# Kernel tuning notes

Measured on AMD Instinct MI355X. Metric: run time of the kernel, lower is better.

Reference implementation:

```python
import jax, jax.numpy as jnp
import numpy as np

D = 128; N_CELLS = 512; N_GENES = 256; HEADS = 4; HD = D // HEADS
E_SP = 8192; E_GRN = 2048

def _ln(x, g, b):
    m = jnp.mean(x, -1, keepdims=True)
    v = jnp.var(x, -1, keepdims=True)
    return (x - m) * jax.lax.rsqrt(v + 1e-5) * g + b

def setup_inputs():
    key = jax.random.key(0)
    ks = jax.random.split(key, 16)
    w = lambda i, shp: jax.random.normal(ks[i], shp, jnp.float32) * 0.02
    return {
        "high_emb": jax.random.normal(ks[0], (N_CELLS, D), jnp.float32),
        "low_emb": jax.random.normal(ks[1], (N_CELLS, N_GENES, D), jnp.float32),
        "spatial_edge_index": jax.random.randint(ks[2], (2, E_SP), 0, N_CELLS),
        "grn_edge_index": jax.random.randint(ks[3], (2, E_GRN), 0, N_GENES),
        "gin_w1": w(4, (D, 2 * D)), "gin_b1": jnp.zeros((2 * D,)),
        "gin_w2": w(5, (2 * D, D)), "gin_b2": jnp.zeros((D,)),
        "gin_eps": jnp.zeros(()),
        "gin_ln_g": jnp.ones((D,)), "gin_ln_b": jnp.zeros((D,)),
        "tc_wq": w(6, (D, D)), "tc_bq": jnp.zeros((D,)),
        "tc_wk": w(7, (D, D)), "tc_bk": jnp.zeros((D,)),
        "tc_wv": w(8, (D, D)), "tc_bv": jnp.zeros((D,)),
        "tc_wskip": w(9, (D, D)), "tc_bskip": jnp.zeros((D,)),
        "tc_ln_g": jnp.ones((D,)), "tc_ln_b": jnp.zeros((D,)),
        "cross_w": w(10, (6, D, D)), "cross_b": jnp.zeros((6, D)),
        "agg_w": w(11, (D, D)), "agg_b": jnp.zeros((D,)),
        "nh_g": jnp.ones((D,)), "nh_b": jnp.zeros((D,)),
        "nl_g": jnp.ones((D,)), "nl_b": jnp.zeros((D,)),
    }

def _forward(high_emb, low_emb, spatial_edge_index, grn_edge_index,
             gin_w1, gin_b1, gin_w2, gin_b2, gin_eps, gin_ln_g, gin_ln_b,
             tc_wq, tc_bq, tc_wk, tc_bk, tc_wv, tc_bv, tc_wskip, tc_bskip,
             tc_ln_g, tc_ln_b, cross_w, cross_b, agg_w, agg_b,
             nh_g, nh_b, nl_g, nl_b):
    # ---- high level: GIN conv over spatial cell graph ----
    s_src, s_dst = spatial_edge_index[0], spatial_edge_index[1]
    agg = jax.ops.segment_sum(high_emb[s_src], s_dst, num_segments=N_CELLS)
    h = (1.0 + gin_eps) * high_emb + agg
    h = jax.nn.gelu(h @ gin_w1 + gin_b1, approximate=False) @ gin_w2 + gin_b2
    high_out = _ln(h, gin_ln_g, gin_ln_b)

    # ---- low level: TransformerConv on per-cell GRN (edge structure shared across cells) ----
    g_src, g_dst = grn_edge_index[0], grn_edge_index[1]
    q = (low_emb @ tc_wq + tc_bq).reshape(N_CELLS, N_GENES, HEADS, HD)
    k = (low_emb @ tc_wk + tc_bk).reshape(N_CELLS, N_GENES, HEADS, HD)
    v = (low_emb @ tc_wv + tc_bv).reshape(N_CELLS, N_GENES, HEADS, HD)
    # per-edge attention logits, edge axis leading for segment ops: (E, C, H)
    logits = jnp.einsum('cehd,cehd->ech', q[:, g_dst], k[:, g_src]) / np.sqrt(HD).astype(np.float32)
    mx = jax.lax.stop_gradient(jax.ops.segment_max(logits, g_dst, num_segments=N_GENES))
    ex = jnp.exp(logits - mx[g_dst])
    den = jax.ops.segment_sum(ex, g_dst, num_segments=N_GENES)
    alpha = ex / den[g_dst]                          # (E, C, H) softmax per target gene
    v_s = jnp.moveaxis(v[:, g_src], 0, 1)            # (E, C, H, HD)
    out = jax.ops.segment_sum(alpha[..., None] * v_s, g_dst, num_segments=N_GENES)
    out = jnp.moveaxis(out, 0, 1).reshape(N_CELLS, N_GENES, D)
    out = out + low_emb @ tc_wskip + tc_bskip        # PyG root_weight skip
    low_out = _ln(out, tc_ln_g, tc_ln_b)

    # ---- gene aggregation + cross-level sigmoid gating ----
    gene_agg = jax.nn.gelu(jnp.mean(low_out, axis=1) @ agg_w + agg_b, approximate=False)
    scale = D ** -0.5
    q1 = high_out @ cross_w[0] + cross_b[0]
    k1 = gene_agg @ cross_w[1] + cross_b[1]
    v1 = gene_agg @ cross_w[2] + cross_b[2]
    high_cross = jax.nn.sigmoid(jnp.sum(q1 * k1, -1, keepdims=True) * scale) * v1
    q2 = gene_agg @ cross_w[3] + cross_b[3]
    k2 = high_out @ cross_w[4] + cross_b[4]
    v2 = high_out @ cross_w[5] + cross_b[5]
    low_cross = jax.nn.sigmoid(jnp.sum(q2 * k2, -1, keepdims=True) * scale) * v2

    high_new = _ln(high_emb + high_out + high_cross, nh_g, nh_b)
    low_new = _ln(low_emb + low_out + low_cross[:, None, :], nl_g, nl_b)
    return (high_new, low_new)

def reference(high_emb, low_emb, spatial_edge_index, grn_edge_index,
              gin_w1, gin_b1, gin_w2, gin_b2, gin_eps, gin_ln_g, gin_ln_b,
              tc_wq, tc_bq, tc_wk, tc_bk, tc_wv, tc_bv, tc_wskip, tc_bskip,
              tc_ln_g, tc_ln_b, cross_w, cross_b, agg_w, agg_b,
              nh_g, nh_b, nl_g, nl_b):
    return _forward(high_emb, low_emb, spatial_edge_index, grn_edge_index,
                    gin_w1, gin_b1, gin_w2, gin_b2, gin_eps, gin_ln_g, gin_ln_b,
                    tc_wq, tc_bq, tc_wk, tc_bk, tc_wv, tc_bv, tc_wskip, tc_bskip,
                    tc_ln_g, tc_ln_b, cross_w, cross_b, agg_w, agg_b,
                    nh_g, nh_b, nl_g, nl_b)
```

## Files before the change

### kernel.cpp

```cpp
#include <hip/hip_runtime.h>
#include <hip/hip_bf16.h>
#include <math.h>

#define N_CELLS 512
#define N_GENES 256
#define D 128
#define HEADS 4
#define HD 32
#define E_SP 8192
#define E_GRN 2048

typedef __attribute__((ext_vector_type(8))) short bf16x8;
typedef __attribute__((ext_vector_type(4))) float f32x4;


__device__ __forceinline__ float gelu_exact(float x) {
    return 0.5f * x * (1.0f + erff(x * 0.70710678118654752f));
}

__device__ __forceinline__ unsigned short f2bf(float f) {
    unsigned u = __float_as_uint(f);
    return (unsigned short)((u + 0x7FFFu + ((u >> 16) & 1u)) >> 16);
}

__device__ __forceinline__ float blo(unsigned u) { return __uint_as_float(u << 16); }
__device__ __forceinline__ float bhi(unsigned u) { return __uint_as_float(u & 0xFFFF0000u); }
__device__ __forceinline__ float bdot(unsigned a, unsigned b) {
    return blo(a) * blo(b) + bhi(a) * bhi(b);
}

template<int NT>
__device__ __forceinline__ float blockSum(float v, float* sbuf) {
    #pragma unroll
    for (int off = 32; off > 0; off >>= 1) v += __shfl_down(v, off, 64);
    int lane = threadIdx.x & 63, wid = threadIdx.x >> 6;
    __syncthreads();
    if (lane == 0) sbuf[wid] = v;
    __syncthreads();
    float r = 0.f;
    #pragma unroll
    for (int i = 0; i < NT / 64; ++i) r += sbuf[i];
    return r;
}


__global__ void gin_scatter_kernel(const float* __restrict__ high,
                                   const int* __restrict__ sp,
                                   float* __restrict__ agg) {
    int tid = blockIdx.x * 256 + threadIdx.x;
    int e = tid >> 7, d = tid & 127;
    int src = sp[e], dst = sp[E_SP + e];
    atomicAdd(&agg[dst * D + d], high[src * D + d]);
}

__global__ __launch_bounds__(256) void gin_mlp_kernel(
    const float* __restrict__ high, const float* __restrict__ agg,
    const float* __restrict__ eps,
    const float* __restrict__ w1, const float* __restrict__ b1,
    const float* __restrict__ w2, const float* __restrict__ b2,
    const float* __restrict__ lng, const float* __restrict__ lnb,
    float* __restrict__ high_out) {
    int c = blockIdx.x;
    int t = threadIdx.x;
    __shared__ float h[D];
    __shared__ float h1[2 * D];
    __shared__ float sbuf[4];
    if (t < D) h[t] = (1.f + eps[0]) * high[c * D + t] + agg[c * D + t];
    __syncthreads();
    float a = b1[t];
    for (int k = 0; k < D; ++k) a += h[k] * w1[k * 256 + t];
    h1[t] = gelu_exact(a);
    __syncthreads();
    float x = 0.f;
    if (t < D) {
        float a2 = b2[t];
        for (int k = 0; k < 256; ++k) a2 += h1[k] * w2[k * D + t];
        x = a2;
    }
    float s = blockSum<256>(x, sbuf);
    float mean = s * (1.f / 128.f);
    float xm = (t < D) ? (x - mean) : 0.f;
    float var = blockSum<256>(xm * xm, sbuf) * (1.f / 128.f);
    if (t < D) high_out[c * D + t] = xm * rsqrtf(var + 1e-5f) * lng[t] + lnb[t];
}


__global__ __launch_bounds__(256) void csr_build_kernel(
    const int* __restrict__ grn,
    int* __restrict__ csr_off, int* __restrict__ csr_eid, int* __restrict__ csr_src) {
    __shared__ int cnt[N_GENES];
    __shared__ int scan[N_GENES];
    __shared__ int cur[N_GENES];
    int t = threadIdx.x;
    cnt[t] = 0;
    __syncthreads();
    for (int e = t; e < E_GRN; e += 256) atomicAdd(&cnt[grn[E_GRN + e]], 1);
    __syncthreads();
    scan[t] = cnt[t];
    __syncthreads();
    #pragma unroll
    for (int s = 1; s < 256; s <<= 1) {
        int v = (t >= s) ? scan[t - s] : 0;
        __syncthreads();
        scan[t] += v;
        __syncthreads();
    }
    int excl = scan[t] - cnt[t];
    csr_off[t] = excl;
    if (t == 255) csr_off[256] = scan[255];
    cur[t] = excl;
    __syncthreads();
    for (int e = t; e < E_GRN; e += 256) {
        int dst = grn[E_GRN + e];
        int pos = atomicAdd(&cur[dst], 1);
        csr_eid[pos] = e;
        csr_src[pos] = grn[e];
    }
}


__global__ __launch_bounds__(256) void wt_kernel(
    const float* __restrict__ wq, const float* __restrict__ wk,
    const float* __restrict__ wv, const float* __restrict__ wskip,
    unsigned short* __restrict__ wt4) {
    __shared__ float tile[128][132];
    int w = blockIdx.x;
    const float* Wp = (w == 0) ? wq : (w == 1) ? wk : (w == 2) ? wv : wskip;
    int t = threadIdx.x;
    #pragma unroll
    for (int rep = 0; rep < 16; ++rep) {
        int f4 = rep * 256 + t;
        float4 v = ((const float4*)Wp)[f4];
        int f = f4 * 4;
        int k = f >> 7, n = f & 127;
        tile[k][n] = v.x; tile[k][n + 1] = v.y; tile[k][n + 2] = v.z; tile[k][n + 3] = v.w;
    }
    __syncthreads();
    unsigned short* out = wt4 + (size_t)w * 16384;
    #pragma unroll
    for (int rep = 0; rep < 16; ++rep) {
        int f4 = rep * 256 + t;
        int f = f4 * 4;
        int n = f >> 7, k = f & 127;
        ushort4 o;
        o.x = f2bf(tile[k][n]);
        o.y = f2bf(tile[k + 1][n]);
        o.z = f2bf(tile[k + 2][n]);
        o.w = f2bf(tile[k + 3][n]);
        *(ushort4*)(out + (size_t)n * 128 + k) = o;
    }
}


__global__ __launch_bounds__(256, 2) void proj4_kernel(
    const float* __restrict__ X,
    const unsigned short* __restrict__ Wt4,
    const float* __restrict__ bq, const float* __restrict__ bk,
    const float* __restrict__ bv, const float* __restrict__ bs,
    unsigned short* __restrict__ Yq, unsigned short* __restrict__ Yk,
    unsigned short* __restrict__ Yv, float* __restrict__ Yskip) {
    __shared__ short Xs[128 * 128];
    __shared__ short Ws[128 * 128];
    int t = threadIdx.x;
    int lane = t & 63, wid = t >> 6;
    const float* Xblk = X + (size_t)blockIdx.x * 128 * 128;

    #pragma unroll
    for (int rep = 0; rep < 16; ++rep) {
        int f4 = rep * 256 + t;
        float4 xv = ((const float4*)Xblk)[f4];
        int f = f4 * 4;
        int row = f >> 7, k = f & 127;
        unsigned p0 = (unsigned)f2bf(xv.x) | ((unsigned)f2bf(xv.y) << 16);
        unsigned p1 = (unsigned)f2bf(xv.z) | ((unsigned)f2bf(xv.w) << 16);
        int eidx = (row * 128 + k) ^ ((row & 7) << 3);
        *(uint2*)(&Xs[eidx]) = make_uint2(p0, p1);
    }

    const float* Bs_[4] = {bq, bk, bv, bs};
    int lr = lane & 15, lg = lane >> 4;
    int rbase = (wid >> 1) * 64, cbase = (wid & 1) * 64;
    int orow0 = blockIdx.x * 128 + rbase;

    for (int w = 0; w < 4; ++w) {
        __syncthreads();
        const uint2* Wsrc = (const uint2*)(Wt4 + (size_t)w * 16384);
        #pragma unroll
        for (int rep = 0; rep < 16; ++rep) {
            int e4 = rep * 256 + t;
            uint2 d2 = Wsrc[e4];
            int f = e4 * 4;
            int n = f >> 7, k = f & 127;
            *(uint2*)(&Ws[(n * 128 + k) ^ ((n & 7) << 3)]) = d2;
        }
        __syncthreads();

        f32x4 acc[4][4] = {};
        #pragma unroll
        for (int ks = 0; ks < 4; ++ks) {
            int k0 = ks * 32 + lg * 8;
            bf16x8 a[4], b[4];
            #pragma unroll
            for (int m = 0; m < 4; ++m) {
                int row = rbase + m * 16 + lr;
                a[m] = *(const bf16x8*)(&Xs[(row * 128 + k0) ^ ((row & 7) << 3)]);
            }
            #pragma unroll
            for (int n = 0; n < 4; ++n) {
                int col = cbase + n * 16 + lr;
                b[n] = *(const bf16x8*)(&Ws[(col * 128 + k0) ^ ((col & 7) << 3)]);
            }
            #pragma unroll
            for (int m = 0; m < 4; ++m)
                #pragma unroll
                for (int n = 0; n < 4; ++n)
                    acc[m][n] = __builtin_amdgcn_mfma_f32_16x16x32_bf16(a[m], b[n], acc[m][n], 0, 0, 0);
        }

        const float* Bb = Bs_[w];
        if (w < 3) {
            unsigned short* Y = (w == 0) ? Yq : (w == 1) ? Yk : Yv;
            #pragma unroll
            for (int n = 0; n < 4; ++n) {
                int col = cbase + n * 16 + lr;
                float bias = Bb[col];
                #pragma unroll
                for (int m = 0; m < 4; ++m)
                    #pragma unroll
                    for (int j = 0; j < 4; ++j) {
                        int row = orow0 + m * 16 + lg * 4 + j;
                        Y[(size_t)row * 128 + col] = f2bf(acc[m][n][j] + bias);
                    }
            }
        } else {
            #pragma unroll
            for (int n = 0; n < 4; ++n) {
                int col = cbase + n * 16 + lr;
                float bias = Bb[col];
                #pragma unroll
                for (int m = 0; m < 4; ++m)
                    #pragma unroll
                    for (int j = 0; j < 4; ++j) {
                        int row = orow0 + m * 16 + lg * 4 + j;
                        Yskip[(size_t)row * 128 + col] = acc[m][n][j] + bias;
                    }
            }
        }
    }
}


__global__ __launch_bounds__(256) void logits_kernel(
    const unsigned short* __restrict__ q, const unsigned short* __restrict__ k,
    const int* __restrict__ grn, float* __restrict__ logits) {
    int c = blockIdx.y;
    int eb = blockIdx.x;
    int t = threadIdx.x;
    int e = eb * 64 + (t >> 2);
    int h = t & 3;
    int src = grn[e], dst = grn[E_GRN + e];
    const unsigned short* qr = q + ((size_t)c * N_GENES + dst) * D + h * HD;
    const unsigned short* kr = k + ((size_t)c * N_GENES + src) * D + h * HD;
    float acc = 0.f;
    #pragma unroll
    for (int i = 0; i < 4; ++i) {
        uint4 qa = *(const uint4*)(qr + i * 8);
        uint4 ka = *(const uint4*)(kr + i * 8);
        acc += bdot(qa.x, ka.x) + bdot(qa.y, ka.y) + bdot(qa.z, ka.z) + bdot(qa.w, ka.w);
    }
    logits[(size_t)c * (E_GRN * 4) + e * 4 + h] = acc * 0.17677669529663687f;
}


__global__ __launch_bounds__(256) void softmax_kernel(
    float* __restrict__ logits,
    const int* __restrict__ csr_off, const int* __restrict__ csr_eid) {
    int c = blockIdx.x;
    int g = threadIdx.x;
    int off = csr_off[g], end = csr_off[g + 1];
    float* base = logits + (size_t)c * (E_GRN * 4);
    float m0 = -1e30f, m1 = -1e30f, m2 = -1e30f, m3 = -1e30f;
    for (int i = off; i < end; ++i) {
        float4 l = *(const float4*)(base + csr_eid[i] * 4);
        m0 = fmaxf(m0, l.x); m1 = fmaxf(m1, l.y); m2 = fmaxf(m2, l.z); m3 = fmaxf(m3, l.w);
    }
    float d0 = 0.f, d1 = 0.f, d2 = 0.f, d3 = 0.f;
    for (int i = off; i < end; ++i) {
        float4 l = *(float4*)(base + csr_eid[i] * 4);
        l.x = expf(l.x - m0); l.y = expf(l.y - m1); l.z = expf(l.z - m2); l.w = expf(l.w - m3);
        d0 += l.x; d1 += l.y; d2 += l.z; d3 += l.w;
        *(float4*)(base + csr_eid[i] * 4) = l;
    }
    float i0 = 1.f / d0, i1 = 1.f / d1, i2 = 1.f / d2, i3 = 1.f / d3;
    for (int i = off; i < end; ++i) {
        float4 l = *(float4*)(base + csr_eid[i] * 4);
        l.x *= i0; l.y *= i1; l.z *= i2; l.w *= i3;
        *(float4*)(base + csr_eid[i] * 4) = l;
    }
}


__global__ __launch_bounds__(128) void pv_ln_kernel(
    const float* __restrict__ alpha, const unsigned short* __restrict__ v,
    const int* __restrict__ csr_off, const int* __restrict__ csr_eid,
    const int* __restrict__ csr_src,
    const float* __restrict__ lng, const float* __restrict__ lnb,
    float* __restrict__ out) {
    int cg = blockIdx.x;
    int c = cg >> 8, g = cg & 255;
    int d = threadIdx.x;
    int h = d >> 5;
    float acc = out[(size_t)cg * D + d];
    int off = csr_off[g], end = csr_off[g + 1];
    const float* ab = alpha + (size_t)c * (E_GRN * 4) + h;
    const unsigned short* vb = v + (size_t)c * N_GENES * D;
    for (int i = off; i < end; ++i) {
        float a = ab[csr_eid[i] * 4];
        acc += a * __uint_as_float((unsigned)vb[(size_t)csr_src[i] * D + d] << 16);
    }
    __shared__ float sbuf[2];
    float s = blockSum<128>(acc, sbuf);
    float mean = s * (1.f / 128.f);
    float xm = acc - mean;
    float var = blockSum<128>(xm * xm, sbuf) * (1.f / 128.f);
    out[(size_t)cg * D + d] = xm * rsqrtf(var + 1e-5f) * lng[d] + lnb[d];
}


__global__ __launch_bounds__(128) void gene_agg_kernel(
    const float* __restrict__ low_out,
    const float* __restrict__ agg_w, const float* __restrict__ agg_b,
    float* __restrict__ gene_agg) {
    int c = blockIdx.x, d = threadIdx.x;
    const float* base = low_out + (size_t)c * N_GENES * D;
    float s = 0.f;
    for (int g = 0; g < N_GENES; ++g) s += base[g * D + d];
    __shared__ float m[D];
    m[d] = s * (1.f / 256.f);
    __syncthreads();
    float acc = agg_b[d];
    for (int k = 0; k < D; ++k) acc += m[k] * agg_w[k * D + d];
    gene_agg[c * D + d] = gelu_exact(acc);
}


__global__ __launch_bounds__(128) void cross_kernel(
    const float* __restrict__ high_emb, const float* __restrict__ high_out,
    const float* __restrict__ gene_agg,
    const float* __restrict__ cw, const float* __restrict__ cb,
    const float* __restrict__ nhg, const float* __restrict__ nhb,
    float* __restrict__ high_new, float* __restrict__ low_cross) {
    int c = blockIdx.x, d = threadIdx.x;
    __shared__ float ho[D], ga[D];
    __shared__ float sbuf[2];
    ho[d] = high_out[c * D + d];
    ga[d] = gene_agg[c * D + d];
    __syncthreads();
    float q1 = cb[0 * D + d], k1 = cb[1 * D + d], v1 = cb[2 * D + d];
    float q2 = cb[3 * D + d], k2 = cb[4 * D + d], v2 = cb[5 * D + d];
    for (int k = 0; k < D; ++k) {
        float hv = ho[k], gv = ga[k];
        q1 += hv * cw[0 * 16384 + k * D + d];
        k1 += gv * cw[1 * 16384 + k * D + d];
        v1 += gv * cw[2 * 16384 + k * D + d];
        q2 += gv * cw[3 * 16384 + k * D + d];
        k2 += hv * cw[4 * 16384 + k * D + d];
        v2 += hv * cw[5 * 16384 + k * D + d];
    }
    const float scale = 0.08838834764831845f;
    float s1 = blockSum<128>(q1 * k1, sbuf);
    float s2 = blockSum<128>(q2 * k2, sbuf);
    float hc = (1.f / (1.f + expf(-s1 * scale))) * v1;
    float lc = (1.f / (1.f + expf(-s2 * scale))) * v2;
    low_cross[c * D + d] = lc;
    float x = high_emb[c * D + d] + ho[d] + hc;
    float sm = blockSum<128>(x, sbuf);
    float mean = sm * (1.f / 128.f);
    float xm = x - mean;
    float var = blockSum<128>(xm * xm, sbuf) * (1.f / 128.f);
    high_new[c * D + d] = xm * rsqrtf(var + 1e-5f) * nhg[d] + nhb[d];
}


__global__ __launch_bounds__(128) void low_final_kernel(
    const float* __restrict__ low_emb, const float* __restrict__ low_cross,
    const float* __restrict__ nlg, const float* __restrict__ nlb,
    float* __restrict__ out) {
    int cg = blockIdx.x;
    int c = cg >> 8;
    int d = threadIdx.x;
    size_t idx = (size_t)cg * D + d;
    float x = low_emb[idx] + out[idx] + low_cross[c * D + d];
    __shared__ float sbuf[2];
    float s = blockSum<128>(x, sbuf);
    float mean = s * (1.f / 128.f);
    float xm = x - mean;
    float var = blockSum<128>(xm * xm, sbuf) * (1.f / 128.f);
    out[idx] = xm * rsqrtf(var + 1e-5f) * nlg[d] + nlb[d];
}


extern "C" void kernel_launch(void* const* d_in, const int* in_sizes, int n_in,
                              void* d_out, int out_size, void* d_ws, size_t ws_size,
                              hipStream_t stream) {
    const float* high_emb = (const float*)d_in[0];
    const float* low_emb  = (const float*)d_in[1];
    const int*   sp       = (const int*)d_in[2];
    const int*   grn      = (const int*)d_in[3];
    const float* gin_w1   = (const float*)d_in[4];
    const float* gin_b1   = (const float*)d_in[5];
    const float* gin_w2   = (const float*)d_in[6];
    const float* gin_b2   = (const float*)d_in[7];
    const float* gin_eps  = (const float*)d_in[8];
    const float* gin_lng  = (const float*)d_in[9];
    const float* gin_lnb  = (const float*)d_in[10];
    const float* tc_wq    = (const float*)d_in[11];
    const float* tc_bq    = (const float*)d_in[12];
    const float* tc_wk    = (const float*)d_in[13];
    const float* tc_bk    = (const float*)d_in[14];
    const float* tc_wv    = (const float*)d_in[15];
    const float* tc_bv    = (const float*)d_in[16];
    const float* tc_wskip = (const float*)d_in[17];
    const float* tc_bskip = (const float*)d_in[18];
    const float* tc_lng   = (const float*)d_in[19];
    const float* tc_lnb   = (const float*)d_in[20];
    const float* cross_w  = (const float*)d_in[21];
    const float* cross_b  = (const float*)d_in[22];
    const float* agg_w    = (const float*)d_in[23];
    const float* agg_b    = (const float*)d_in[24];
    const float* nh_g     = (const float*)d_in[25];
    const float* nh_b     = (const float*)d_in[26];
    const float* nl_g     = (const float*)d_in[27];
    const float* nl_b     = (const float*)d_in[28];

    float* out = (float*)d_out;
    float* out_high = out;
    float* out_low  = out + N_CELLS * D;

    const size_t LOW_N = (size_t)N_CELLS * N_GENES * D;

    unsigned short* q_b = (unsigned short*)d_ws;
    unsigned short* k_b = q_b + LOW_N;
    unsigned short* v_b = k_b + LOW_N;
    float* ws_logits    = (float*)(v_b + LOW_N);
    float* ws_agg       = ws_logits + (size_t)N_CELLS * E_GRN * HEADS;
    float* ws_high_out  = ws_agg + N_CELLS * D;
    float* ws_gene_agg  = ws_high_out + N_CELLS * D;
    float* ws_low_cross = ws_gene_agg + N_CELLS * D;
    unsigned short* wt4 = (unsigned short*)(ws_low_cross + N_CELLS * D);
    int* csr_off = (int*)(wt4 + 4 * 128 * 128);
    int* csr_eid = csr_off + 260;
    int* csr_src = csr_eid + E_GRN;

    hipMemsetAsync(ws_agg, 0, N_CELLS * D * sizeof(float), stream);
    gin_scatter_kernel<<<E_SP * D / 256, 256, 0, stream>>>(high_emb, sp, ws_agg);
    gin_mlp_kernel<<<N_CELLS, 256, 0, stream>>>(high_emb, ws_agg, gin_eps,
        gin_w1, gin_b1, gin_w2, gin_b2, gin_lng, gin_lnb, ws_high_out);

    csr_build_kernel<<<1, N_GENES, 0, stream>>>(grn, csr_off, csr_eid, csr_src);
    wt_kernel<<<4, 256, 0, stream>>>(tc_wq, tc_wk, tc_wv, tc_wskip, wt4);

    proj4_kernel<<<N_CELLS * N_GENES / 128, 256, 0, stream>>>(
        low_emb, wt4, tc_bq, tc_bk, tc_bv, tc_bskip, q_b, k_b, v_b, out_low);

    logits_kernel<<<dim3(E_GRN / 64, N_CELLS), 256, 0, stream>>>(q_b, k_b, grn, ws_logits);
    softmax_kernel<<<N_CELLS, N_GENES, 0, stream>>>(ws_logits, csr_off, csr_eid);

    pv_ln_kernel<<<N_CELLS * N_GENES, 128, 0, stream>>>(
        ws_logits, v_b, csr_off, csr_eid, csr_src, tc_lng, tc_lnb, out_low);

    gene_agg_kernel<<<N_CELLS, 128, 0, stream>>>(out_low, agg_w, agg_b, ws_gene_agg);

    cross_kernel<<<N_CELLS, 128, 0, stream>>>(high_emb, ws_high_out, ws_gene_agg,
        cross_w, cross_b, nh_g, nh_b, out_high, ws_low_cross);

    low_final_kernel<<<N_CELLS * N_GENES, 128, 0, stream>>>(
        low_emb, ws_low_cross, nl_g, nl_b, out_low);
}
```

Before: 545.9 us.

## Fuse GRN attention logits, softmax and aggregation into one per-cell kernel

Replaces the separate logits, softmax and PV+layernorm kernels with a single per-cell kernel that stages K, then V, for the cell in LDS and keeps attention weights in shared memory, removing the global logits buffer round trips. Also replaces the atomic scatter for the GIN aggregation with a CSR built over spatial edges and a gather inside the GIN MLP kernel. The cost is one 512-thread block per cell with 96KB of dynamic LDS, which limits occupancy to 512 blocks total, and serial per-edge wave reductions.

```diff
diff --git a/kernel.cpp b/kernel.cpp
--- a/kernel.cpp
+++ b/kernel.cpp
@@ -44,17 +44,75 @@
 }
 
 
-__global__ void gin_scatter_kernel(const float* __restrict__ high,
-                                   const int* __restrict__ sp,
-                                   float* __restrict__ agg) {
-    int tid = blockIdx.x * 256 + threadIdx.x;
-    int e = tid >> 7, d = tid & 127;
-    int src = sp[e], dst = sp[E_SP + e];
-    atomicAdd(&agg[dst * D + d], high[src * D + d]);
-}
+__global__ __launch_bounds__(512) void sp_csr_kernel(const int* __restrict__ sp,
+                                                     int* __restrict__ sp_off,
+                                                     int* __restrict__ sp_src) {
+    __shared__ int cnt[512];
+    __shared__ int scan[512];
+    __shared__ int cur[512];
+    int t = threadIdx.x;
+    cnt[t] = 0;
+    __syncthreads();
+    for (int e = t; e < E_SP; e += 512) atomicAdd(&cnt[sp[E_SP + e]], 1);
+    __syncthreads();
+    scan[t] = cnt[t];
+    __syncthreads();
+    #pragma unroll
+    for (int s = 1; s < 512; s <<= 1) {
+        int v = (t >= s) ? scan[t - s] : 0;
+        __syncthreads();
+        scan[t] += v;
+        __syncthreads();
+    }
+    int excl = scan[t] - cnt[t];
+    sp_off[t] = excl;
+    if (t == 511) sp_off[512] = scan[511];
+    cur[t] = excl;
+    __syncthreads();
+    for (int e = t; e < E_SP; e += 512) {
+        int dst = sp[E_SP + e];
+        int pos = atomicAdd(&cur[dst], 1);
+        sp_src[pos] = sp[e];
+    }
+}
+
+
+__global__ __launch_bounds__(256) void gene_csr_kernel(const int* __restrict__ grn,
+                                                       int* __restrict__ csr_off,
+                                                       int* __restrict__ csr_src) {
+    __shared__ int cnt[N_GENES];
+    __shared__ int scan[N_GENES];
+    __shared__ int cur[N_GENES];
+    int t = threadIdx.x;
+    cnt[t] = 0;
+    __syncthreads();
+    for (int e = t; e < E_GRN; e += 256) atomicAdd(&cnt[grn[E_GRN + e]], 1);
+    __syncthreads();
+    scan[t] = cnt[t];
+    __syncthreads();
+    #pragma unroll
+    for (int s = 1; s < 256; s <<= 1) {
+        int v = (t >= s) ? scan[t - s] : 0;
+        __syncthreads();
+        scan[t] += v;
+        __syncthreads();
+    }
+    int excl = scan[t] - cnt[t];
+    csr_off[t] = excl;
+    if (t == 255) csr_off[256] = scan[255];
+    cur[t] = excl;
+    __syncthreads();
+    for (int e = t; e < E_GRN; e += 256) {
+        int dst = grn[E_GRN + e];
+        int pos = atomicAdd(&cur[dst], 1);
+        csr_src[pos] = grn[e];
+    }
+}
+
 
 __global__ __launch_bounds__(256) void gin_mlp_kernel(
-    const float* __restrict__ high, const float* __restrict__ agg,
+    const float* __restrict__ high,
+    const int* __restrict__ sp_off, const int* __restrict__ sp_src,
     const float* __restrict__ eps,
     const float* __restrict__ w1, const float* __restrict__ b1,
     const float* __restrict__ w2, const float* __restrict__ b2,
@@ -65,7 +123,12 @@
     __shared__ float h[D];
     __shared__ float h1[2 * D];
     __shared__ float sbuf[4];
-    if (t < D) h[t] = (1.f + eps[0]) * high[c * D + t] + agg[c * D + t];
+    if (t < D) {
+        float acc = 0.f;
+        int off = sp_off[c], end = sp_off[c + 1];
+        for (int i = off; i < end; ++i) acc += high[(size_t)sp_src[i] * D + t];
+        h[t] = (1.f + eps[0]) * high[c * D + t] + acc;
+    }
     __syncthreads();
     float a = b1[t];
     for (int k = 0; k < D; ++k) a += h[k] * w1[k * 256 + t];
@@ -82,40 +145,6 @@
     float xm = (t < D) ? (x - mean) : 0.f;
     float var = blockSum<256>(xm * xm, sbuf) * (1.f / 128.f);
     if (t < D) high_out[c * D + t] = xm * rsqrtf(var + 1e-5f) * lng[t] + lnb[t];
-}
-
-
-__global__ __launch_bounds__(256) void csr_build_kernel(
-    const int* __restrict__ grn,
-    int* __restrict__ csr_off, int* __restrict__ csr_eid, int* __restrict__ csr_src) {
-    __shared__ int cnt[N_GENES];
-    __shared__ int scan[N_GENES];
-    __shared__ int cur[N_GENES];
-    int t = threadIdx.x;
-    cnt[t] = 0;
-    __syncthreads();
-    for (int e = t; e < E_GRN; e += 256) atomicAdd(&cnt[grn[E_GRN + e]], 1);
-    __syncthreads();
-    scan[t] = cnt[t];
-    __syncthreads();
-    #pragma unroll
-    for (int s = 1; s < 256; s <<= 1) {
-        int v = (t >= s) ? scan[t - s] : 0;
-        __syncthreads();
-        scan[t] += v;
-        __syncthreads();
-    }
-    int excl = scan[t] - cnt[t];
-    csr_off[t] = excl;
-    if (t == 255) csr_off[256] = scan[255];
-    cur[t] = excl;
-    __syncthreads();
-    for (int e = t; e < E_GRN; e += 256) {
-        int dst = grn[E_GRN + e];
-        int pos = atomicAdd(&cur[dst], 1);
-        csr_eid[pos] = e;
-        csr_src[pos] = grn[e];
-    }
 }
 
 
@@ -250,80 +279,105 @@
 }
 
 
-__global__ __launch_bounds__(256) void logits_kernel(
+__global__ __launch_bounds__(512) void attn_fused_kernel(
     const unsigned short* __restrict__ q, const unsigned short* __restrict__ k,
-    const int* __restrict__ grn, float* __restrict__ logits) {
-    int c = blockIdx.y;
-    int eb = blockIdx.x;
-    int t = threadIdx.x;
-    int e = eb * 64 + (t >> 2);
-    int h = t & 3;
-    int src = grn[e], dst = grn[E_GRN + e];
-    const unsigned short* qr = q + ((size_t)c * N_GENES + dst) * D + h * HD;
-    const unsigned short* kr = k + ((size_t)c * N_GENES + src) * D + h * HD;
-    float acc = 0.f;
-    #pragma unroll
-    for (int i = 0; i < 4; ++i) {
-        uint4 qa = *(const uint4*)(qr + i * 8);
-        uint4 ka = *(const uint4*)(kr + i * 8);
-        acc += bdot(qa.x, ka.x) + bdot(qa.y, ka.y) + bdot(qa.z, ka.z) + bdot(qa.w, ka.w);
-    }
-    logits[(size_t)c * (E_GRN * 4) + e * 4 + h] = acc * 0.17677669529663687f;
-}
-
-
-__global__ __launch_bounds__(256) void softmax_kernel(
-    float* __restrict__ logits,
-    const int* __restrict__ csr_off, const int* __restrict__ csr_eid) {
-    int c = blockIdx.x;
-    int g = threadIdx.x;
-    int off = csr_off[g], end = csr_off[g + 1];
-    float* base = logits + (size_t)c * (E_GRN * 4);
-    float m0 = -1e30f, m1 = -1e30f, m2 = -1e30f, m3 = -1e30f;
-    for (int i = off; i < end; ++i) {
-        float4 l = *(const float4*)(base + csr_eid[i] * 4);
-        m0 = fmaxf(m0, l.x); m1 = fmaxf(m1, l.y); m2 = fmaxf(m2, l.z); m3 = fmaxf(m3, l.w);
-    }
-    float d0 = 0.f, d1 = 0.f, d2 = 0.f, d3 = 0.f;
-    for (int i = off; i < end; ++i) {
-        float4 l = *(float4*)(base + csr_eid[i] * 4);
-        l.x = expf(l.x - m0); l.y = expf(l.y - m1); l.z = expf(l.z - m2); l.w = expf(l.w - m3);
-        d0 += l.x; d1 += l.y; d2 += l.z; d3 += l.w;
-        *(float4*)(base + csr_eid[i] * 4) = l;
-    }
-    float i0 = 1.f / d0, i1 = 1.f / d1, i2 = 1.f / d2, i3 = 1.f / d3;
-    for (int i = off; i < end; ++i) {
-        float4 l = *(float4*)(base + csr_eid[i] * 4);
-        l.x *= i0; l.y *= i1; l.z *= i2; l.w *= i3;
-        *(float4*)(base + csr_eid[i] * 4) = l;
-    }
-}
-
-
-__global__ __launch_bounds__(128) void pv_ln_kernel(
-    const float* __restrict__ alpha, const unsigned short* __restrict__ v,
-    const int* __restrict__ csr_off, const int* __restrict__ csr_eid,
-    const int* __restrict__ csr_src,
+    const unsigned short* __restrict__ v,
+    const int* __restrict__ csr_off, const int* __restrict__ csr_src,
     const float* __restrict__ lng, const float* __restrict__ lnb,
     float* __restrict__ out) {
-    int cg = blockIdx.x;
-    int c = cg >> 8, g = cg & 255;
-    int d = threadIdx.x;
-    int h = d >> 5;
-    float acc = out[(size_t)cg * D + d];
-    int off = csr_off[g], end = csr_off[g + 1];
-    const float* ab = alpha + (size_t)c * (E_GRN * 4) + h;
-    const unsigned short* vb = v + (size_t)c * N_GENES * D;
-    for (int i = off; i < end; ++i) {
-        float a = ab[csr_eid[i] * 4];
-        acc += a * __uint_as_float((unsigned)vb[(size_t)csr_src[i] * D + d] << 16);
-    }
-    __shared__ float sbuf[2];
-    float s = blockSum<128>(acc, sbuf);
-    float mean = s * (1.f / 128.f);
-    float xm = acc - mean;
-    float var = blockSum<128>(xm * xm, sbuf) * (1.f / 128.f);
-    out[(size_t)cg * D + d] = xm * rsqrtf(var + 1e-5f) * lng[d] + lnb[d];
+    extern __shared__ char smem[];
+    unsigned short* kv = (unsigned short*)smem;
+    float* alpha = (float*)(smem + 65536);
+    int c = blockIdx.x;
+    int t = threadIdx.x, lane = t & 63, wid = t >> 6;
+    int h = lane >> 4, r = lane & 15;
+    const size_t cbase = (size_t)c * N_GENES * D;
+
+    {
+        const uint4* s4 = (const uint4*)(k + cbase);
+        uint4* d4 = (uint4*)kv;
+        #pragma unroll
+        for (int i = 0; i < 8; ++i) d4[i * 512 + t] = s4[i * 512 + t];
+    }
+    __syncthreads();
+
+    uint qv_next = *(const uint*)(q + cbase + (size_t)wid * D + 2 * lane);
+    for (int it = 0; it < 32; ++it) {
+        int g = it * 8 + wid;
+        uint qv = qv_next;
+        if (it < 31)
+            qv_next = *(const uint*)(q + cbase + (size_t)(g + 8) * D + 2 * lane);
+        int off = csr_off[g], end = csr_off[g + 1];
+        for (int i = off; i < end; ++i) {
+            int sg = csr_src[i];
+            uint kk = *(const uint*)(kv + sg * D + 2 * lane);
+            float p = bdot(qv, kk);
+            p += __shfl_xor(p, 1);
+            p += __shfl_xor(p, 2);
+            p += __shfl_xor(p, 4);
+            p += __shfl_xor(p, 8);
+            if (r == 0) alpha[i * 4 + h] = p * 0.17677669529663687f;
+        }
+        float m = -1e30f;
+        for (int i = off + r; i < end; i += 16) m = fmaxf(m, alpha[i * 4 + h]);
+        m = fmaxf(m, __shfl_xor(m, 1));
+        m = fmaxf(m, __shfl_xor(m, 2));
+        m = fmaxf(m, __shfl_xor(m, 4));
+        m = fmaxf(m, __shfl_xor(m, 8));
+        float s = 0.f;
+        for (int i = off + r; i < end; i += 16) {
+            float e = expf(alpha[i * 4 + h] - m);
+            alpha[i * 4 + h] = e;
+            s += e;
+        }
+        s += __shfl_xor(s, 1);
+        s += __shfl_xor(s, 2);
+        s += __shfl_xor(s, 4);
+        s += __shfl_xor(s, 8);
+        float inv = 1.f / s;
+        for (int i = off + r; i < end; i += 16) alpha[i * 4 + h] *= inv;
+    }
+    __syncthreads();
+
+    {
+        const uint4* s4 = (const uint4*)(v + cbase);
+        uint4* d4 = (uint4*)kv;
+        #pragma unroll
+        for (int i = 0; i < 8; ++i) d4[i * 512 + t] = s4[i * 512 + t];
+    }
+    __syncthreads();
+
+    float2 lg = *(const float2*)(lng + 2 * lane);
+    float2 lb = *(const float2*)(lnb + 2 * lane);
+    float2 sk_next = *(const float2*)(out + cbase + (size_t)wid * D + 2 * lane);
+    for (int it = 0; it < 32; ++it) {
+        int g = it * 8 + wid;
+        float ax = sk_next.x, ay = sk_next.y;
+        if (it < 31)
+            sk_next = *(const float2*)(out + cbase + (size_t)(g + 8) * D + 2 * lane);
+        int off = csr_off[g], end = csr_off[g + 1];
+        for (int i = off; i < end; ++i) {
+            float a = alpha[i * 4 + h];
+            int sg = csr_src[i];
+            uint vv = *(const uint*)(kv + sg * D + 2 * lane);
+            ax += a * blo(vv);
+            ay += a * bhi(vv);
+        }
+        float s = ax + ay;
+        s += __shfl_xor(s, 1);  s += __shfl_xor(s, 2);  s += __shfl_xor(s, 4);
+        s += __shfl_xor(s, 8);  s += __shfl_xor(s, 16); s += __shfl_xor(s, 32);
+        float mean = s * (1.f / 128.f);
+        float dx = ax - mean, dy = ay - mean;
+        float vs = dx * dx + dy * dy;
+        vs += __shfl_xor(vs, 1);  vs += __shfl_xor(vs, 2);  vs += __shfl_xor(vs, 4);
+        vs += __shfl_xor(vs, 8);  vs += __shfl_xor(vs, 16); vs += __shfl_xor(vs, 32);
+        float var = vs * (1.f / 128.f);
+        float rs = rsqrtf(var + 1e-5f);
+        float2 o;
+        o.x = dx * rs * lg.x + lb.x;
+        o.y = dy * rs * lg.y + lb.y;
+        *(float2*)(out + cbase + (size_t)g * D + 2 * lane) = o;
+    }
 }
 
 
@@ -442,32 +496,27 @@
     unsigned short* q_b = (unsigned short*)d_ws;
     unsigned short* k_b = q_b + LOW_N;
     unsigned short* v_b = k_b + LOW_N;
-    float* ws_logits    = (float*)(v_b + LOW_N);
-    float* ws_agg       = ws_logits + (size_t)N_CELLS * E_GRN * HEADS;
-    float* ws_high_out  = ws_agg + N_CELLS * D;
+    float* ws_high_out  = (float*)(v_b + LOW_N);
     float* ws_gene_agg  = ws_high_out + N_CELLS * D;
     float* ws_low_cross = ws_gene_agg + N_CELLS * D;
     unsigned short* wt4 = (unsigned short*)(ws_low_cross + N_CELLS * D);
     int* csr_off = (int*)(wt4 + 4 * 128 * 128);
-    int* csr_eid = csr_off + 260;
-    int* csr_src = csr_eid + E_GRN;
-
-    hipMemsetAsync(ws_agg, 0, N_CELLS * D * sizeof(float), stream);
-    gin_scatter_kernel<<<E_SP * D / 256, 256, 0, stream>>>(high_emb, sp, ws_agg);
-    gin_mlp_kernel<<<N_CELLS, 256, 0, stream>>>(high_emb, ws_agg, gin_eps,
+    int* csr_src = csr_off + 260;
+    int* sp_off  = csr_src + E_GRN;
+    int* sp_src  = sp_off + 516;
+
+    sp_csr_kernel<<<1, 512, 0, stream>>>(sp, sp_off, sp_src);
+    gene_csr_kernel<<<1, 256, 0, stream>>>(grn, csr_off, csr_src);
+    wt_kernel<<<4, 256, 0, stream>>>(tc_wq, tc_wk, tc_wv, tc_wskip, wt4);
+
+    gin_mlp_kernel<<<N_CELLS, 256, 0, stream>>>(high_emb, sp_off, sp_src, gin_eps,
         gin_w1, gin_b1, gin_w2, gin_b2, gin_lng, gin_lnb, ws_high_out);
-
-    csr_build_kernel<<<1, N_GENES, 0, stream>>>(grn, csr_off, csr_eid, csr_src);
-    wt_kernel<<<4, 256, 0, stream>>>(tc_wq, tc_wk, tc_wv, tc_wskip, wt4);
 
     proj4_kernel<<<N_CELLS * N_GENES / 128, 256, 0, stream>>>(
         low_emb, wt4, tc_bq, tc_bk, tc_bv, tc_bskip, q_b, k_b, v_b, out_low);
 
-    logits_kernel<<<dim3(E_GRN / 64, N_CELLS), 256, 0, stream>>>(q_b, k_b, grn, ws_logits);
-    softmax_kernel<<<N_CELLS, N_GENES, 0, stream>>>(ws_logits, csr_off, csr_eid);
-
-    pv_ln_kernel<<<N_CELLS * N_GENES, 128, 0, stream>>>(
-        ws_logits, v_b, csr_off, csr_eid, csr_src, tc_lng, tc_lnb, out_low);
+    attn_fused_kernel<<<N_CELLS, 512, 98304, stream>>>(
+        q_b, k_b, v_b, csr_off, csr_src, tc_lng, tc_lnb, out_low);
 
     gene_agg_kernel<<<N_CELLS, 128, 0, stream>>>(out_low, agg_w, agg_b, ws_gene_agg);
 
```

Measured after the change: 696.2 us. +27.5%, slower.
